# Optimization experiments

Hardware: AMD Instinct MI355X
Metric: run time of the kernel (lower is better)

The kernel has to match this reference:

```python
import jax, jax.numpy as jnp
import numpy as np

N_NODES = 100000
N_EDGES = 1250000
D_FEAT = 64


def setup_inputs() -> dict:
    key = jax.random.key(0)
    kx, ke = jax.random.split(key)
    x = jax.random.normal(kx, (N_NODES, D_FEAT), dtype=jnp.float32)
    edge_index = jax.random.randint(ke, (2, N_EDGES), 0, N_NODES, dtype=jnp.int64)
    return {"x": x, "edge_index": edge_index}


def reference(x, edge_index):
    # adj[src, dst] = 1; x_neighbors = adj.T @ x  ->
    # x_neighbors[i] = sum_{edges (s, d) with d == i} x[s]
    src, dst = edge_index[0], edge_index[1]
    msgs = x[src]  # [n_edges, d_feat] gather
    x_neighbors = jax.ops.segment_sum(msgs, dst, num_segments=x.shape[0])
    return x_neighbors
```

## Files before the change

### kernel.cpp

```cpp
#include <hip/hip_runtime.h>
#include <hip/hip_bf16.h>

#define N_NODES 100000
#define N_EDGES 1250000
#define D_FEAT  64
#define BKT_NODES 64
#define NB      1563
#define CAP     1024
#define OVF_CAP 8192
#define EPB_I4  1024
#define N_I4    (N_EDGES / 4)
#define NBLK_BUILD ((N_I4 + EPB_I4 - 1) / EPB_I4)

__global__ __launch_bounds__(256) void to_bf16(
    const float* __restrict__ x, ushort* __restrict__ xh)
{
    int t = blockIdx.x * 256 + threadIdx.x;
    const float4* x4 = (const float4*)x;
    float4 a = x4[2 * t];
    float4 b = x4[2 * t + 1];
    float f[8] = {a.x, a.y, a.z, a.w, b.x, b.y, b.z, b.w};
    uint h[8];
#pragma unroll
    for (int i = 0; i < 8; ++i) {
        uint u = __float_as_uint(f[i]);
        u += 0x7FFFu + ((u >> 16) & 1u);
        h[i] = u >> 16;
    }
    uint4 o;
    o.x = h[0] | (h[1] << 16);
    o.y = h[2] | (h[3] << 16);
    o.z = h[4] | (h[5] << 16);
    o.w = h[6] | (h[7] << 16);
    ((uint4*)xh)[t] = o;
}

__global__ __launch_bounds__(256) void build_buckets(
    const int* __restrict__ src, const int* __restrict__ dst,
    uint* __restrict__ fill, uint* __restrict__ pairs,
    uint* __restrict__ ovfCnt, int2* __restrict__ ovf)
{
    __shared__ uint cnt[NB];
    __shared__ uint base[NB];
    const int t = threadIdx.x;
    for (int i = t; i < NB; i += 256) cnt[i] = 0;
    __syncthreads();

    uint   pw[16];
    ushort pb[16];
    ushort pr[16];
    bool   vk[4];
    const int i40 = blockIdx.x * EPB_I4;
#pragma unroll
    for (int k = 0; k < 4; ++k) {
        int i4 = i40 + t + k * 256;
        vk[k] = (i4 < N_I4);
        if (vk[k]) {
            int4 d4 = ((const int4*)dst)[i4];
            int4 s4 = ((const int4*)src)[i4];
            int dd[4] = {d4.x, d4.y, d4.z, d4.w};
            int ss[4] = {s4.x, s4.y, s4.z, s4.w};
#pragma unroll
            for (int j = 0; j < 4; ++j) {
                uint b = ((uint)dd[j]) >> 6;
                uint r = atomicAdd(&cnt[b], 1u);
                pw[k * 4 + j] = ((((uint)dd[j]) & 63u) << 17) | (uint)ss[j];
                pb[k * 4 + j] = (ushort)b;
                pr[k * 4 + j] = (ushort)r;
            }
        }
    }
    __syncthreads();

    for (int i = t; i < NB; i += 256) {
        uint c = cnt[i];
        base[i] = c ? atomicAdd(&fill[i], c) : 0u;
    }
    __syncthreads();

#pragma unroll
    for (int j = 0; j < 16; ++j) {
        if (vk[j >> 2]) {
            uint b = pb[j];
            uint g = base[b] + pr[j];
            if (g < CAP) {
                pairs[(size_t)b * CAP + g] = pw[j];
            } else {
                uint o = atomicAdd(ovfCnt, 1u);
                if (o < OVF_CAP)
                    ovf[o] = make_int2((int)(pw[j] & 0x1FFFFu),
                                       (int)((b << 6) | (pw[j] >> 17)));
            }
        }
    }
}

__global__ __launch_bounds__(256) void bucket_aggregate(
    const ushort* __restrict__ xh, const uint* __restrict__ pairs,
    const uint* __restrict__ fill, float* __restrict__ out)
{
    __shared__ uint pw[CAP];
    __shared__ uint srt[CAP];
    __shared__ int  cnt[BKT_NODES];
    __shared__ int  scn[BKT_NODES];
    __shared__ int  basea[BKT_NODES];
    __shared__ int  pos[BKT_NODES];

    const int t = threadIdx.x;
    const int b = blockIdx.x;
    const int n = min((int)fill[b], CAP);

    if (t < BKT_NODES) cnt[t] = 0;
    __syncthreads();
    for (int i = t; i < n; i += 256) {
        uint w = pairs[(size_t)b * CAP + i];
        pw[i] = w;
        atomicAdd(&cnt[w >> 17], 1);
    }
    __syncthreads();

    if (t < BKT_NODES) scn[t] = cnt[t];
    __syncthreads();
    for (int off = 1; off < BKT_NODES; off <<= 1) {
        int v = (t < BKT_NODES && t >= off) ? scn[t - off] : 0;
        __syncthreads();
        if (t < BKT_NODES) scn[t] += v;
        __syncthreads();
    }
    if (t < BKT_NODES) { int e = scn[t] - cnt[t]; basea[t] = e; pos[t] = e; }
    __syncthreads();

    for (int i = t; i < n; i += 256) {
        uint w = pw[i];
        int r = atomicAdd(&pos[w >> 17], 1);
        srt[r] = w & 0x1FFFFu;
    }
    __syncthreads();

    const int wid  = t >> 6;
    const int lane = t & 63;
    const int sub  = lane >> 3;
    const int l8   = lane & 7;
    const uint4* __restrict__ xrow = (const uint4*)xh;

    for (int nl = wid; nl < BKT_NODES; nl += 4) {
        const int node  = b * BKT_NODES + nl;
        const int start = basea[nl];
        const int deg   = cnt[nl];

        float f[8];
#pragma unroll
        for (int j = 0; j < 8; ++j) f[j] = 0.f;

        int i = sub;
        for (; i + 8 < deg; i += 16) {
            uint s0 = srt[start + i];
            uint s1 = srt[start + i + 8];
            uint4 v0 = xrow[(size_t)s0 * 8 + l8];
            uint4 v1 = xrow[(size_t)s1 * 8 + l8];
            f[0] += __uint_as_float((v0.x & 0xFFFFu) << 16);
            f[1] += __uint_as_float(v0.x & 0xFFFF0000u);
            f[2] += __uint_as_float((v0.y & 0xFFFFu) << 16);
            f[3] += __uint_as_float(v0.y & 0xFFFF0000u);
            f[4] += __uint_as_float((v0.z & 0xFFFFu) << 16);
            f[5] += __uint_as_float(v0.z & 0xFFFF0000u);
            f[6] += __uint_as_float((v0.w & 0xFFFFu) << 16);
            f[7] += __uint_as_float(v0.w & 0xFFFF0000u);
            f[0] += __uint_as_float((v1.x & 0xFFFFu) << 16);
            f[1] += __uint_as_float(v1.x & 0xFFFF0000u);
            f[2] += __uint_as_float((v1.y & 0xFFFFu) << 16);
            f[3] += __uint_as_float(v1.y & 0xFFFF0000u);
            f[4] += __uint_as_float((v1.z & 0xFFFFu) << 16);
            f[5] += __uint_as_float(v1.z & 0xFFFF0000u);
            f[6] += __uint_as_float((v1.w & 0xFFFFu) << 16);
            f[7] += __uint_as_float(v1.w & 0xFFFF0000u);
        }
        if (i < deg) {
            uint s0 = srt[start + i];
            uint4 v0 = xrow[(size_t)s0 * 8 + l8];
            f[0] += __uint_as_float((v0.x & 0xFFFFu) << 16);
            f[1] += __uint_as_float(v0.x & 0xFFFF0000u);
            f[2] += __uint_as_float((v0.y & 0xFFFFu) << 16);
            f[3] += __uint_as_float(v0.y & 0xFFFF0000u);
            f[4] += __uint_as_float((v0.z & 0xFFFFu) << 16);
            f[5] += __uint_as_float(v0.z & 0xFFFF0000u);
            f[6] += __uint_as_float((v0.w & 0xFFFFu) << 16);
            f[7] += __uint_as_float(v0.w & 0xFFFF0000u);
        }

#pragma unroll
        for (int j = 0; j < 8; ++j) {
            f[j] += __shfl_xor(f[j], 8, 64);
            f[j] += __shfl_xor(f[j], 16, 64);
            f[j] += __shfl_xor(f[j], 32, 64);
        }

        if (lane < 8 && node < N_NODES) {
            float4* out4 = (float4*)out;
            out4[(size_t)node * 16 + l8 * 2]     = make_float4(f[0], f[1], f[2], f[3]);
            out4[(size_t)node * 16 + l8 * 2 + 1] = make_float4(f[4], f[5], f[6], f[7]);
        }
    }
}

__global__ __launch_bounds__(256) void ovf_fixup(
    const float* __restrict__ x, const int2* __restrict__ ovf,
    const uint* __restrict__ ovfCnt, float* __restrict__ out)
{
    const int n = min((int)*ovfCnt, OVF_CAP);
    const int wave = (blockIdx.x * blockDim.x + threadIdx.x) >> 6;
    const int lane = threadIdx.x & 63;
    const int nwaves = (gridDim.x * blockDim.x) >> 6;
    for (int e = wave; e < n; e += nwaves) {
        int2 p = ovf[e];
        atomicAdd(&out[(size_t)p.y * D_FEAT + lane], x[(size_t)p.x * D_FEAT + lane]);
    }
}

extern "C" void kernel_launch(void* const* d_in, const int* in_sizes, int n_in,
                              void* d_out, int out_size, void* d_ws, size_t ws_size,
                              hipStream_t stream) {
    const float* x = (const float*)d_in[0];
    const int* edge_index = (const int*)d_in[1];
    const int* src = edge_index;
    const int* dst = edge_index + N_EDGES;
    float* out = (float*)d_out;

    ushort* xh     = (ushort*)d_ws;
    uint*   pairs  = (uint*)(xh + (size_t)N_NODES * D_FEAT);
    uint*   fill   = pairs + (size_t)NB * CAP;
    uint*   ovfCnt = fill + NB;
    int2*   ovf    = (int2*)(fill + NB + 3);

    hipMemsetAsync(fill, 0, (NB + 3) * sizeof(uint), stream);

    to_bf16<<<(N_NODES * D_FEAT / 8) / 256, 256, 0, stream>>>(x, xh);
    build_buckets<<<NBLK_BUILD, 256, 0, stream>>>(src, dst, fill, pairs, ovfCnt, ovf);
    bucket_aggregate<<<NB, 256, 0, stream>>>(xh, pairs, fill, out);
    ovf_fixup<<<16, 256, 0, stream>>>(x, ovf, ovfCnt, out);
}
```

Baseline: 147.2 us.

## Split bucketing into coarse super-buckets, in-place CSR repartition, and separate gather

Replaces 64-node buckets with 512-node super-buckets, which cuts the per-block shared counters and global fill atomics in the build phase. A new repart kernel sorts each super-bucket in place by destination and writes per-node offset/degree words. A separate gather kernel then reads sources from global memory instead of shared memory. This adds one kernel launch and an extra global round trip for the sorted indices. The larger bucket capacity makes overflow less likely.

```diff
diff --git a/kernel.cpp b/kernel.cpp
--- a/kernel.cpp
+++ b/kernel.cpp
@@ -4,13 +4,15 @@
 #define N_NODES 100000
 #define N_EDGES 1250000
 #define D_FEAT  64
-#define BKT_NODES 64
-#define NB      1563
-#define CAP     1024
+#define SB_NODES 512
+#define SB_SHIFT 9
+#define NSB     196
+#define CAP_SB  7040
 #define OVF_CAP 8192
 #define EPB_I4  1024
 #define N_I4    (N_EDGES / 4)
 #define NBLK_BUILD ((N_I4 + EPB_I4 - 1) / EPB_I4)
+#define RT      512
 
 __global__ __launch_bounds__(256) void to_bf16(
     const float* __restrict__ x, ushort* __restrict__ xh)
@@ -35,15 +37,15 @@
     ((uint4*)xh)[t] = o;
 }
 
-__global__ __launch_bounds__(256) void build_buckets(
+__global__ __launch_bounds__(256) void build_sb(
     const int* __restrict__ src, const int* __restrict__ dst,
     uint* __restrict__ fill, uint* __restrict__ pairs,
     uint* __restrict__ ovfCnt, int2* __restrict__ ovf)
 {
-    __shared__ uint cnt[NB];
-    __shared__ uint base[NB];
+    __shared__ uint cnt[NSB];
+    __shared__ uint base[NSB];
     const int t = threadIdx.x;
-    for (int i = t; i < NB; i += 256) cnt[i] = 0;
+    for (int i = t; i < NSB; i += 256) cnt[i] = 0;
     __syncthreads();
 
     uint   pw[16];
@@ -62,9 +64,9 @@
             int ss[4] = {s4.x, s4.y, s4.z, s4.w};
 #pragma unroll
             for (int j = 0; j < 4; ++j) {
-                uint b = ((uint)dd[j]) >> 6;
+                uint b = ((uint)dd[j]) >> SB_SHIFT;
                 uint r = atomicAdd(&cnt[b], 1u);
-                pw[k * 4 + j] = ((((uint)dd[j]) & 63u) << 17) | (uint)ss[j];
+                pw[k * 4 + j] = ((((uint)dd[j]) & (SB_NODES - 1u)) << 17) | (uint)ss[j];
                 pb[k * 4 + j] = (ushort)b;
                 pr[k * 4 + j] = (ushort)r;
             }
@@ -72,7 +74,7 @@
     }
     __syncthreads();
 
-    for (int i = t; i < NB; i += 256) {
+    for (int i = t; i < NSB; i += 256) {
         uint c = cnt[i];
         base[i] = c ? atomicAdd(&fill[i], c) : 0u;
     }
@@ -83,70 +85,80 @@
         if (vk[j >> 2]) {
             uint b = pb[j];
             uint g = base[b] + pr[j];
-            if (g < CAP) {
-                pairs[(size_t)b * CAP + g] = pw[j];
+            if (g < CAP_SB) {
+                pairs[(size_t)b * CAP_SB + g] = pw[j];
             } else {
                 uint o = atomicAdd(ovfCnt, 1u);
                 if (o < OVF_CAP)
                     ovf[o] = make_int2((int)(pw[j] & 0x1FFFFu),
-                                       (int)((b << 6) | (pw[j] >> 17)));
+                                       (int)((b << SB_SHIFT) | (pw[j] >> 17)));
             }
         }
     }
 }
 
-__global__ __launch_bounds__(256) void bucket_aggregate(
-    const ushort* __restrict__ xh, const uint* __restrict__ pairs,
-    const uint* __restrict__ fill, float* __restrict__ out)
-{
-    __shared__ uint pw[CAP];
-    __shared__ uint srt[CAP];
-    __shared__ int  cnt[BKT_NODES];
-    __shared__ int  scn[BKT_NODES];
-    __shared__ int  basea[BKT_NODES];
-    __shared__ int  pos[BKT_NODES];
-
-    const int t = threadIdx.x;
-    const int b = blockIdx.x;
-    const int n = min((int)fill[b], CAP);
-
-    if (t < BKT_NODES) cnt[t] = 0;
-    __syncthreads();
-    for (int i = t; i < n; i += 256) {
-        uint w = pairs[(size_t)b * CAP + i];
+__global__ __launch_bounds__(RT) void repart(
+    uint* __restrict__ pairs, const uint* __restrict__ fill,
+    uint* __restrict__ offs)
+{
+    __shared__ uint pw[CAP_SB];
+    __shared__ int  cnt[SB_NODES];
+    __shared__ int  scn[SB_NODES];
+    __shared__ int  pos[SB_NODES];
+
+    const int t  = threadIdx.x;
+    const int sb = blockIdx.x;
+    const int n  = min((int)fill[sb], CAP_SB);
+    const size_t base = (size_t)sb * CAP_SB;
+
+    cnt[t] = 0;
+    __syncthreads();
+    for (int i = t; i < n; i += RT) {
+        uint w = pairs[base + i];
         pw[i] = w;
         atomicAdd(&cnt[w >> 17], 1);
     }
     __syncthreads();
 
-    if (t < BKT_NODES) scn[t] = cnt[t];
-    __syncthreads();
-    for (int off = 1; off < BKT_NODES; off <<= 1) {
-        int v = (t < BKT_NODES && t >= off) ? scn[t - off] : 0;
+    scn[t] = cnt[t];
+    __syncthreads();
+    for (int off = 1; off < SB_NODES; off <<= 1) {
+        int v = (t >= off) ? scn[t - off] : 0;
         __syncthreads();
-        if (t < BKT_NODES) scn[t] += v;
+        scn[t] += v;
         __syncthreads();
     }
-    if (t < BKT_NODES) { int e = scn[t] - cnt[t]; basea[t] = e; pos[t] = e; }
-    __syncthreads();
-
-    for (int i = t; i < n; i += 256) {
+    {
+        int e = scn[t] - cnt[t];
+        pos[t] = e;
+        offs[sb * SB_NODES + t] = (uint)e | ((uint)cnt[t] << 16);
+    }
+    __syncthreads();
+
+    for (int i = t; i < n; i += RT) {
         uint w = pw[i];
         int r = atomicAdd(&pos[w >> 17], 1);
-        srt[r] = w & 0x1FFFFu;
-    }
-    __syncthreads();
-
+        pairs[base + r] = w & 0x1FFFFu;
+    }
+}
+
+__global__ __launch_bounds__(256) void gather_csr(
+    const ushort* __restrict__ xh, const uint* __restrict__ pairs,
+    const uint* __restrict__ offs, float* __restrict__ out)
+{
+    const int t    = threadIdx.x;
     const int wid  = t >> 6;
     const int lane = t & 63;
     const int sub  = lane >> 3;
     const int l8   = lane & 7;
     const uint4* __restrict__ xrow = (const uint4*)xh;
 
-    for (int nl = wid; nl < BKT_NODES; nl += 4) {
-        const int node  = b * BKT_NODES + nl;
-        const int start = basea[nl];
-        const int deg   = cnt[nl];
+    for (int nl = wid; nl < 64; nl += 4) {
+        const int node = blockIdx.x * 64 + nl;
+        if (node >= N_NODES) break;
+        const uint v    = offs[node];
+        const int start = (node >> SB_SHIFT) * CAP_SB + (int)(v & 0xFFFFu);
+        const int deg   = (int)(v >> 16);
 
         float f[8];
 #pragma unroll
@@ -154,8 +166,8 @@
 
         int i = sub;
         for (; i + 8 < deg; i += 16) {
-            uint s0 = srt[start + i];
-            uint s1 = srt[start + i + 8];
+            uint s0 = pairs[start + i];
+            uint s1 = pairs[start + i + 8];
             uint4 v0 = xrow[(size_t)s0 * 8 + l8];
             uint4 v1 = xrow[(size_t)s1 * 8 + l8];
             f[0] += __uint_as_float((v0.x & 0xFFFFu) << 16);
@@ -176,7 +188,7 @@
             f[7] += __uint_as_float(v1.w & 0xFFFF0000u);
         }
         if (i < deg) {
-            uint s0 = srt[start + i];
+            uint s0 = pairs[start + i];
             uint4 v0 = xrow[(size_t)s0 * 8 + l8];
             f[0] += __uint_as_float((v0.x & 0xFFFFu) << 16);
             f[1] += __uint_as_float(v0.x & 0xFFFF0000u);
@@ -195,7 +207,7 @@
             f[j] += __shfl_xor(f[j], 32, 64);
         }
 
-        if (lane < 8 && node < N_NODES) {
+        if (lane < 8) {
             float4* out4 = (float4*)out;
             out4[(size_t)node * 16 + l8 * 2]     = make_float4(f[0], f[1], f[2], f[3]);
             out4[(size_t)node * 16 + l8 * 2 + 1] = make_float4(f[4], f[5], f[6], f[7]);
@@ -228,14 +240,16 @@
 
     ushort* xh     = (ushort*)d_ws;
     uint*   pairs  = (uint*)(xh + (size_t)N_NODES * D_FEAT);
-    uint*   fill   = pairs + (size_t)NB * CAP;
-    uint*   ovfCnt = fill + NB;
-    int2*   ovf    = (int2*)(fill + NB + 3);
-
-    hipMemsetAsync(fill, 0, (NB + 3) * sizeof(uint), stream);
+    uint*   offs   = pairs + (size_t)NSB * CAP_SB;
+    uint*   fill   = offs + NSB * SB_NODES;
+    uint*   ovfCnt = fill + NSB;
+    int2*   ovf    = (int2*)(fill + NSB + 2);
+
+    hipMemsetAsync(fill, 0, (NSB + 2) * sizeof(uint), stream);
 
     to_bf16<<<(N_NODES * D_FEAT / 8) / 256, 256, 0, stream>>>(x, xh);
-    build_buckets<<<NBLK_BUILD, 256, 0, stream>>>(src, dst, fill, pairs, ovfCnt, ovf);
-    bucket_aggregate<<<NB, 256, 0, stream>>>(xh, pairs, fill, out);
+    build_sb<<<NBLK_BUILD, 256, 0, stream>>>(src, dst, fill, pairs, ovfCnt, ovf);
+    repart<<<NSB, RT, 0, stream>>>(pairs, fill, offs);
+    gather_csr<<<(N_NODES + 63) / 64, 256, 0, stream>>>(xh, pairs, offs, out);
     ovf_fixup<<<16, 256, 0, stream>>>(x, ovf, ovfCnt, out);
 }
```

New measurement: 155.0 us. 5.3% more time.
